# Performance work log

Measured on AMD Instinct MI355X. Metric: run time of the kernel, lower is better.

## Reference

```python
import jax, jax.numpy as jnp
import numpy as np

D_MODEL = 4096
D_HEAD = 128
N_ROPES = 4096
ROPE_COEF = 1.0


def _rope_buffers(n_ropes, d_head, rope_coef):
    # Faithful to torch _get_rotary_vectors (including the (i-1) exponent and
    # sin[:, 1::2] = cos(m) quirk).
    i = jnp.arange(d_head // 2, dtype=jnp.float32)
    theta = 10000.0 ** (-2.0 * (i - 1.0) / d_head)          # [d_head/2]
    m = jnp.arange(n_ropes, dtype=jnp.float32)[:, None] * theta * rope_coef  # [P, d/2]
    cosm, sinm = jnp.cos(m), jnp.sin(m)
    cos = jnp.repeat(cosm, 2, axis=-1)                       # even & odd = cos(m)
    sin = jnp.stack([-sinm, cosm], axis=-1).reshape(n_ropes, d_head)  # even=-sin, odd=cos
    return sin, cos


def setup_inputs() -> dict:
    key = jax.random.key(0)
    ks = jax.random.split(key, 7)
    x = jax.random.normal(ks[0], (4, 4096, D_MODEL), dtype=jnp.float32)
    w_q = jax.random.normal(ks[1], (D_HEAD, D_MODEL), dtype=jnp.float32) * 0.02
    w_k = jax.random.normal(ks[2], (D_HEAD, D_MODEL), dtype=jnp.float32) * 0.02
    w_v = jax.random.normal(ks[3], (D_HEAD, D_MODEL), dtype=jnp.float32) * 0.02
    b_q = jax.random.normal(ks[4], (D_HEAD,), dtype=jnp.float32) * 0.02
    b_k = jax.random.normal(ks[5], (D_HEAD,), dtype=jnp.float32) * 0.02
    b_v = jax.random.normal(ks[6], (D_HEAD,), dtype=jnp.float32) * 0.02
    sin, cos = _rope_buffers(N_ROPES, D_HEAD, ROPE_COEF)
    return {"x": x, "w_q": w_q, "b_q": b_q, "w_k": w_k, "b_k": b_k,
            "w_v": w_v, "b_v": b_v, "sin": sin, "cos": cos}


def reference(x, w_q, b_q, w_k, b_k, w_v, b_v, sin, cos):
    b, seq_len, d_model = x.shape
    q = jnp.einsum('bsd,hd->bsh', x, w_q) + b_q   # [B,S,d_head]
    k = jnp.einsum('bsd,hd->bsh', x, w_k) + b_k
    v = jnp.einsum('bsd,hd->bsh', x, w_v) + b_v
    c, s = cos[:seq_len], sin[:seq_len]
    # Torch in-place aliased swap puts the original ODD values into both
    # even and odd slots: [o0,o0,o1,o1,...].
    q_sw = jnp.repeat(q[..., 1::2], 2, axis=-1)
    k_sw = jnp.repeat(k[..., 1::2], 2, axis=-1)
    q_rot = q * c + q_sw * s
    k_rot = k * c + k_sw * s
    # causal scaled-dot-product attention (q/k/v are [B,S,d_head])
    scale = 1.0 / jnp.sqrt(jnp.float32(q.shape[-1]))
    scores = jnp.einsum('bqh,bkh->bqk', q_rot, k_rot) * scale
    causal = jnp.tril(jnp.ones((seq_len, seq_len), dtype=bool))
    scores = jnp.where(causal, scores, jnp.finfo(scores.dtype).min)
    attn = jax.nn.softmax(scores, axis=-1)
    return jnp.einsum('bqk,bkh->bqh', attn, v)
```

## Files before the change

kernel.cpp:

```cpp
#include <hip/hip_runtime.h>
#include <hip/hip_bf16.h>
#include <float.h>
#include <math.h>

typedef float f32x4 __attribute__((ext_vector_type(4)));
typedef short short8 __attribute__((ext_vector_type(8)));
typedef unsigned int uint32;

#define NB 4
#define SQ 4096
#define DM 4096
#define DH 128
#define LOG2E 1.44269504088896f
#define SCALE 0.0883883476483184f
#define SCL2 (SCALE * LOG2E)

__device__ __forceinline__ unsigned short f2bf(float f) {
  union { float f; unsigned u; } x; x.f = f;
  unsigned r = x.u + 0x7FFFu + ((x.u >> 16) & 1u);
  return (unsigned short)(r >> 16);
}

__device__ __forceinline__ uint2 cvt4(float4 f) {
  uint2 u;
  asm("v_cvt_pk_bf16_f32 %0, %1, %2" : "=v"(u.x) : "v"(f.x), "v"(f.y));
  asm("v_cvt_pk_bf16_f32 %0, %1, %2" : "=v"(u.y) : "v"(f.z), "v"(f.w));
  return u;
}

#define GLD16(g, l) __builtin_amdgcn_global_load_lds( \
    (const __attribute__((address_space(1))) void*)(g), \
    (__attribute__((address_space(3))) void*)(l), 16, 0, 0)

__global__ void cast_w_kernel(const float* __restrict__ wq, const float* __restrict__ wk,
                              const float* __restrict__ wv, const float* __restrict__ bq,
                              const float* __restrict__ bk, const float* __restrict__ bv,
                              unsigned short* __restrict__ wb, float* __restrict__ biasws) {
  int t = blockIdx.x * 256 + threadIdx.x;
  int base = t * 8;
  int n = base >> 12;
  int d = base & 4095;
  const float* src = (n < 128) ? (wq + (size_t)n * DM)
                   : (n < 256) ? (wk + (size_t)(n - 128) * DM)
                               : (wv + (size_t)(n - 256) * DM);
  float4 f0 = *(const float4*)(src + d);
  float4 f1 = *(const float4*)(src + d + 4);
  short8 v;
  v[0] = (short)f2bf(f0.x); v[1] = (short)f2bf(f0.y);
  v[2] = (short)f2bf(f0.z); v[3] = (short)f2bf(f0.w);
  v[4] = (short)f2bf(f1.x); v[5] = (short)f2bf(f1.y);
  v[6] = (short)f2bf(f1.z); v[7] = (short)f2bf(f1.w);
  *(short8*)(wb + base) = v;
  if (t < 384) biasws[t] = (t < 128) ? bq[t] : (t < 256) ? bk[t - 128] : bv[t - 256];
}

__global__ __launch_bounds__(256) void gemm_qkv_rope(
    const float* __restrict__ x, const unsigned short* __restrict__ wb,
    const float* __restrict__ biasws, const float* __restrict__ sing,
    const float* __restrict__ cosg, unsigned short* __restrict__ qb,
    unsigned short* __restrict__ kb, unsigned short* __restrict__ vt) {
  __shared__ __align__(16) short Alds[2 * 64 * 64];
  __shared__ __align__(16) short Blds[2 * 128 * 64];
  const int tid = threadIdx.x;
  const int l = tid & 63, w = tid >> 6;
  const int wm = w >> 1, wn = w & 1;
  const int l15 = l & 15, lg = l >> 4;
  const int bid = blockIdx.x;
  const int xcd = bid & 7, j = bid >> 3;
  const int mloc = j / 3, head = j - mloc * 3;
  const int m0 = (xcd * 32 + mloc) * 64;
  f32x4 acc[2][4] = {};
  const int ar0 = tid >> 4, ac4 = (tid & 15) * 4;
  const float* xsrc = x + (size_t)(m0 + ar0) * DM + ac4;
  const int achunk = (tid & 15) >> 1, ahalf = tid & 1;
  const int brow_ = tid >> 3, bchunk = tid & 7;
  const unsigned short* wbh = wb + (size_t)head * 128 * DM;
  float4 a00, a01, a02, a03, a10, a11, a12, a13;
  {
#pragma unroll
    for (int i = 0; i < 4; ++i) {
      float4 f = *(const float4*)(xsrc + (size_t)i * 16 * DM);
      int row = ar0 + i * 16;
      *(uint2*)&Alds[row * 64 + ((achunk ^ (row & 7)) * 8) + ahalf * 4] = cvt4(f);
    }
#pragma unroll
    for (int i = 0; i < 4; ++i) {
      int row = i * 32 + brow_;
      int slot = i * 256 + tid;
      GLD16(wbh + (size_t)row * DM + ((bchunk ^ (row & 7)) * 8), (char*)Blds + slot * 16);
    }
    a00 = *(const float4*)(xsrc + 64);
    a01 = *(const float4*)(xsrc + (size_t)16 * DM + 64);
    a02 = *(const float4*)(xsrc + (size_t)32 * DM + 64);
    a03 = *(const float4*)(xsrc + (size_t)48 * DM + 64);
  }
  auto giter = [&](int t, int CUR,
                   float4& n0, float4& n1, float4& n2, float4& n3,
                   float4& f0, float4& f1, float4& f2, float4& f3) {
    asm volatile("s_waitcnt vmcnt(4) lgkmcnt(0)" ::: "memory");
    __builtin_amdgcn_sched_barrier(0);
    __builtin_amdgcn_s_barrier();
    __builtin_amdgcn_sched_barrier(0);
    const int kB = (t + 1) * 64;
    char* bdst = (char*)Blds + (CUR ^ 1) * 16384;
#pragma unroll
    for (int i = 0; i < 4; ++i) {
      int row = i * 32 + brow_;
      int slot = i * 256 + tid;
      GLD16(wbh + (size_t)row * DM + kB + ((bchunk ^ (row & 7)) * 8), bdst + slot * 16);
    }
    __builtin_amdgcn_sched_barrier(0);
    const int kF = (t < 62) ? (t + 2) * 64 : 0;
    f0 = *(const float4*)(xsrc + kF);
    f1 = *(const float4*)(xsrc + (size_t)16 * DM + kF);
    f2 = *(const float4*)(xsrc + (size_t)32 * DM + kF);
    f3 = *(const float4*)(xsrc + (size_t)48 * DM + kF);
#pragma unroll
    for (int kc = 0; kc < 2; ++kc) {
      short8 af[2], bfr[4];
#pragma unroll
      for (int mi = 0; mi < 2; ++mi) {
        int r = wm * 32 + mi * 16 + l15;
        af[mi] = *(short8*)&Alds[CUR * 4096 + r * 64 + ((kc * 32 + lg * 8) ^ ((r & 7) << 3))];
      }
#pragma unroll
      for (int ni = 0; ni < 4; ++ni) {
        int r = wn * 64 + ni * 16 + l15;
        bfr[ni] = *(short8*)&Blds[CUR * 8192 + r * 64 + ((kc * 32 + lg * 8) ^ ((r & 7) << 3))];
      }
#pragma unroll
      for (int mi = 0; mi < 2; ++mi)
#pragma unroll
        for (int ni = 0; ni < 4; ++ni)
          acc[mi][ni] = __builtin_amdgcn_mfma_f32_16x16x32_bf16(af[mi], bfr[ni], acc[mi][ni], 0, 0, 0);
    }
    short* Adst = &Alds[(CUR ^ 1) * 4096];
    int r0 = ar0, r1 = ar0 + 16, r2 = ar0 + 32, r3 = ar0 + 48;
    *(uint2*)&Adst[r0 * 64 + ((achunk ^ (r0 & 7)) * 8) + ahalf * 4] = cvt4(n0);
    *(uint2*)&Adst[r1 * 64 + ((achunk ^ (r1 & 7)) * 8) + ahalf * 4] = cvt4(n1);
    *(uint2*)&Adst[r2 * 64 + ((achunk ^ (r2 & 7)) * 8) + ahalf * 4] = cvt4(n2);
    *(uint2*)&Adst[r3 * 64 + ((achunk ^ (r3 & 7)) * 8) + ahalf * 4] = cvt4(n3);
  };
#pragma unroll 1
  for (int t = 0; t < 62; t += 2) {
    giter(t, 0, a00, a01, a02, a03, a10, a11, a12, a13);
    giter(t + 1, 1, a10, a11, a12, a13, a00, a01, a02, a03);
  }
  giter(62, 0, a00, a01, a02, a03, a10, a11, a12, a13);
  {
    asm volatile("s_waitcnt vmcnt(0) lgkmcnt(0)" ::: "memory");
    __builtin_amdgcn_sched_barrier(0);
    __builtin_amdgcn_s_barrier();
    __builtin_amdgcn_sched_barrier(0);
#pragma unroll
    for (int kc = 0; kc < 2; ++kc) {
      short8 af[2], bfr[4];
#pragma unroll
      for (int mi = 0; mi < 2; ++mi) {
        int r = wm * 32 + mi * 16 + l15;
        af[mi] = *(short8*)&Alds[4096 + r * 64 + ((kc * 32 + lg * 8) ^ ((r & 7) << 3))];
      }
#pragma unroll
      for (int ni = 0; ni < 4; ++ni) {
        int r = wn * 64 + ni * 16 + l15;
        bfr[ni] = *(short8*)&Blds[8192 + r * 64 + ((kc * 32 + lg * 8) ^ ((r & 7) << 3))];
      }
#pragma unroll
      for (int mi = 0; mi < 2; ++mi)
#pragma unroll
        for (int ni = 0; ni < 4; ++ni)
          acc[mi][ni] = __builtin_amdgcn_mfma_f32_16x16x32_bf16(af[mi], bfr[ni], acc[mi][ni], 0, 0, 0);
    }
  }
  if (head == 2) {
    unsigned short* vtb = vt + (size_t)(m0 >> 12) * DH * SQ;
    const int srow = (m0 & (SQ - 1)) + wm * 32;
#pragma unroll
    for (int mi = 0; mi < 2; ++mi)
#pragma unroll
      for (int ni = 0; ni < 4; ++ni) {
        int h = wn * 64 + ni * 16 + l15;
        float bias = biasws[256 + h];
        f32x4 a = acc[mi][ni];
        float4 f;
        f.x = a[0] + bias; f.y = a[1] + bias; f.z = a[2] + bias; f.w = a[3] + bias;
        *(uint2*)&vtb[(size_t)h * SQ + srow + mi * 16 + lg * 4] = cvt4(f);
      }
  } else {
    unsigned short* dst = (head == 0) ? qb : kb;
#pragma unroll
    for (int mi = 0; mi < 2; ++mi)
#pragma unroll
      for (int ni = 0; ni < 4; ++ni) {
        int h = wn * 64 + ni * 16 + l15;
        float bias = biasws[head * 128 + h];
        f32x4 a = acc[mi][ni];
#pragma unroll
        for (int j2 = 0; j2 < 4; ++j2) {
          int row = m0 + wm * 32 + mi * 16 + lg * 4 + j2;
          float val = a[j2] + bias;
          int s = row & (SQ - 1);
          float cs = cosg[s * DH + h];
          float sn = sing[s * DH + h];
          float pr = __shfl_xor(val, 1, 64);
          float sw = (l & 1) ? val : pr;
          val = val * cs + sw * sn;
          dst[(size_t)row * DH + h] = f2bf(val);
        }
      }
  }
}

__global__ __launch_bounds__(256) void attn_kernel(
    const unsigned short* __restrict__ qb, const unsigned short* __restrict__ kb,
    const unsigned short* __restrict__ vt, float* __restrict__ out) {
  __shared__ __align__(16) short KV[4 * 8192];
  __shared__ __align__(16) short Plds4[4 * 1152];
  __shared__ __align__(16) float Mlds[64];
  __shared__ __align__(16) float Llds[64];
  __shared__ __align__(16) float Clds[64];
  const int tid = threadIdx.x;
  const int w = tid >> 6, l = tid & 63;
  const int qsub = w >> 1, ksp = w & 1;
  const int l15 = l & 15, lg = l >> 4;

  const int bi = blockIdx.x;
  const int slot = bi & 7, p5 = slot & 1, batch = slot >> 1;
  const int a = bi >> 3;
  const int t = (a & 1) ? (127 - p5 * 32 - (a >> 1)) : (p5 * 32 + (a >> 1));
  const int q0 = t * 32;
  const int qb0 = q0 + qsub * 16;
  const size_t bbase = (size_t)batch * SQ;
  const unsigned short* Kb = kb + bbase * DH;
  const unsigned short* Vtb = vt + (size_t)batch * DH * SQ;

  short* Kp = KV + ksp * 8192;
  short* Vp = KV + 16384 + ksp * 8192;
  short* Pw = Plds4 + w * 1152;

  const int ti = qsub * 64 + l;
  const int krow_ = ti >> 4, kc_ = ti & 15;
  const int vrow_ = ti >> 3, vc_ = ti & 7;

  short8 qf[4];
  {
    const unsigned short* qp = qb + (bbase + qb0 + l15) * DH + lg * 8;
#pragma unroll
    for (int kcd = 0; kcd < 4; ++kcd) qf[kcd] = *(const short8*)(qp + kcd * 32);
  }

  const int nsteps = (q0 + 32 + 63) >> 6;
  const int nsteps_w = (qb0 + 16 + 63) >> 6;
  const int max_nit = (nsteps + 1) >> 1;

  float m_r = -INFINITY, l_r = 0.f;
  f32x4 o[8] = {};

  for (int it = 0; it < max_nit; ++it) {
    const int st = it * 2 + ksp;
    const int kv0 = st * 64;
    if (st < nsteps) {
#pragma unroll
      for (int i = 0; i < 8; ++i) {
        int row = i * 8 + krow_;
        GLD16(Kb + (size_t)(kv0 + row) * DH + ((kc_ ^ (row & 15)) * 8),
              (char*)Kp + (i * 128 + ti) * 16);
      }
#pragma unroll
      for (int i = 0; i < 8; ++i) {
        int row = i * 16 + vrow_;
        GLD16(Vtb + (size_t)row * SQ + kv0 + ((vc_ ^ (row & 7)) * 8),
              (char*)Vp + (i * 128 + ti) * 16);
      }
    }
    asm volatile("s_waitcnt vmcnt(0)" ::: "memory");
    __builtin_amdgcn_s_barrier();

    if (st < nsteps_w) {
      f32x4 sf[4] = {};
      __builtin_amdgcn_s_setprio(1);
#pragma unroll
      for (int kcd = 0; kcd < 4; ++kcd)
#pragma unroll
        for (int ni = 0; ni < 4; ++ni) {
          int r = ni * 16 + l15;
          short8 kf = *(short8*)&Kp[r * 128 + (((kcd * 4 + lg) ^ (r & 15)) * 8)];
          sf[ni] = __builtin_amdgcn_mfma_f32_16x16x32_bf16(kf, qf[kcd], sf[ni], 0, 0, 0);
        }
      __builtin_amdgcn_s_setprio(0);

      float s[4][4];
      if (st == nsteps_w - 1) {
#pragma unroll
        for (int ni = 0; ni < 4; ++ni)
#pragma unroll
          for (int j = 0; j < 4; ++j) {
            float v = sf[ni][j] * SCL2;
            if (kv0 + ni * 16 + lg * 4 + j > qb0 + l15) v = -FLT_MAX;
            s[ni][j] = v;
          }
      } else {
#pragma unroll
        for (int ni = 0; ni < 4; ++ni)
#pragma unroll
          for (int j = 0; j < 4; ++j) s[ni][j] = sf[ni][j] * SCL2;
      }

      float tmx = s[0][0];
#pragma unroll
      for (int ni = 0; ni < 4; ++ni)
#pragma unroll
        for (int j = 0; j < 4; ++j) tmx = fmaxf(tmx, s[ni][j]);
      tmx = fmaxf(tmx, __shfl_xor(tmx, 16, 64));
      tmx = fmaxf(tmx, __shfl_xor(tmx, 32, 64));

      if (__any(tmx > m_r + 8.0f)) {
        float mnew = fmaxf(m_r, tmx);
        float corr = exp2f(m_r - mnew);
        if (l < 16) Clds[w * 16 + l] = corr;
        l_r *= corr; m_r = mnew;
        f32x4 c4 = *(f32x4*)&Clds[w * 16 + lg * 4];
#pragma unroll
        for (int nd = 0; nd < 8; ++nd)
#pragma unroll
          for (int j = 0; j < 4; ++j) o[nd][j] *= c4[j];
      }

      float rs = 0.f;
      float pp[4][4];
#pragma unroll
      for (int ni = 0; ni < 4; ++ni)
#pragma unroll
        for (int j = 0; j < 4; ++j) {
          pp[ni][j] = exp2f(s[ni][j] - m_r);
          rs += pp[ni][j];
        }
      rs += __shfl_xor(rs, 16, 64);
      rs += __shfl_xor(rs, 32, 64);
      l_r += rs;

#pragma unroll
      for (int ni = 0; ni < 4; ++ni) {
        uint32 lo, hi;
        asm volatile("v_cvt_pk_bf16_f32 %0, %1, %2" : "=v"(lo) : "v"(pp[ni][0]), "v"(pp[ni][1]));
        asm volatile("v_cvt_pk_bf16_f32 %0, %1, %2" : "=v"(hi) : "v"(pp[ni][2]), "v"(pp[ni][3]));
        uint2 u; u.x = lo; u.y = hi;
        *(uint2*)&Pw[l15 * 72 + ni * 16 + lg * 4] = u;
      }
      short8 pa0 = *(short8*)&Pw[l15 * 72 + lg * 8];
      short8 pa1 = *(short8*)&Pw[l15 * 72 + 32 + lg * 8];

      __builtin_amdgcn_s_setprio(1);
#pragma unroll
      for (int nd = 0; nd < 8; ++nd) {
        int r = nd * 16 + l15;
        short8 v0 = *(short8*)&Vp[r * 64 + ((lg ^ (r & 7)) * 8)];
        short8 v1 = *(short8*)&Vp[r * 64 + (((lg + 4) ^ (r & 7)) * 8)];
        o[nd] = __builtin_amdgcn_mfma_f32_16x16x32_bf16(pa0, v0, o[nd], 0, 0, 0);
        o[nd] = __builtin_amdgcn_mfma_f32_16x16x32_bf16(pa1, v1, o[nd], 0, 0, 0);
      }
      __builtin_amdgcn_s_setprio(0);
    }
    __builtin_amdgcn_s_barrier();
  }

  if (l < 16) { Mlds[w * 16 + l] = m_r; Llds[w * 16 + l] = l_r; }
  __syncthreads();
  float* Ob = (float*)KV;
#pragma unroll
  for (int nd = 0; nd < 8; ++nd)
#pragma unroll
    for (int j = 0; j < 4; ++j)
      Ob[w * 2112 + (lg * 4 + j) * 132 + nd * 16 + l15] = o[nd][j];
  __syncthreads();
  {
    const int w0 = qsub * 2, w1 = qsub * 2 + 1;
    float al0[4], al1[4], Lt[4];
#pragma unroll
    for (int j = 0; j < 4; ++j) {
      int q = lg * 4 + j;
      float ma = Mlds[w0 * 16 + q], mb = Mlds[w1 * 16 + q];
      float M = fmaxf(ma, mb);
      al0[j] = exp2f(ma - M); al1[j] = exp2f(mb - M);
      Lt[j] = al0[j] * Llds[w0 * 16 + q] + al1[j] * Llds[w1 * 16 + q];
    }
#pragma unroll
    for (int t2 = 0; t2 < 4; ++t2) {
      int nd = ksp * 4 + t2;
#pragma unroll
      for (int j = 0; j < 4; ++j) {
        int q = lg * 4 + j;
        float acc2 = al0[j] * Ob[w0 * 2112 + q * 132 + nd * 16 + l15]
                   + al1[j] * Ob[w1 * 2112 + q * 132 + nd * 16 + l15];
        out[(bbase + qb0 + q) * DH + nd * 16 + l15] = acc2 / Lt[j];
      }
    }
  }
}

extern "C" void kernel_launch(void* const* d_in, const int* in_sizes, int n_in,
                              void* d_out, int out_size, void* d_ws, size_t ws_size,
                              hipStream_t stream) {
  const float* x    = (const float*)d_in[0];
  const float* wq   = (const float*)d_in[1];
  const float* bq   = (const float*)d_in[2];
  const float* wk   = (const float*)d_in[3];
  const float* bk   = (const float*)d_in[4];
  const float* wv   = (const float*)d_in[5];
  const float* bv   = (const float*)d_in[6];
  const float* sing = (const float*)d_in[7];
  const float* cosg = (const float*)d_in[8];
  float* out = (float*)d_out;

  char* ws = (char*)d_ws;
  unsigned short* wb = (unsigned short*)ws;
  float* biasws = (float*)(ws + 3145728);
  unsigned short* qb = (unsigned short*)(ws + 3147264);
  unsigned short* kb = (unsigned short*)(ws + 3147264 + 4194304);
  unsigned short* vt = (unsigned short*)(ws + 3147264 + 2 * 4194304);

  cast_w_kernel<<<768, 256, 0, stream>>>(wq, wk, wv, bq, bk, bv, wb, biasws);
  gemm_qkv_rope<<<768, 256, 0, stream>>>(x, wb, biasws, sing, cosg, qb, kb, vt);
  attn_kernel<<<512, 256, 0, stream>>>(qb, kb, vt, out);
}
```

Before: 177.0 us.

## Rewrite QKV GEMM to load fragments directly from global into registers without LDS

The QKV projection GEMM drops its LDS double-buffered tiles. Each wave now loads its A (fp32 x) and B (bf16 weight) MFMA fragments straight from global memory into a three-deep register ring, converting A to bf16 in registers. The grid becomes 1536 blocks of 128 threads, each covering 128 rows by 32 output columns, with no block barriers. This is meant to remove LDS traffic and synchronisation, but it raises register pressure and global/L2 traffic because tiles are no longer shared across waves.

```diff
diff --git a/kernel.cpp b/kernel.cpp
--- a/kernel.cpp
+++ b/kernel.cpp
@@ -26,6 +26,17 @@
   asm("v_cvt_pk_bf16_f32 %0, %1, %2" : "=v"(u.x) : "v"(f.x), "v"(f.y));
   asm("v_cvt_pk_bf16_f32 %0, %1, %2" : "=v"(u.y) : "v"(f.z), "v"(f.w));
   return u;
+}
+
+__device__ __forceinline__ short8 pack8(f32x4 u, f32x4 v) {
+  uint32 r0, r1, r2, r3;
+  asm("v_cvt_pk_bf16_f32 %0, %1, %2" : "=v"(r0) : "v"(u[0]), "v"(u[1]));
+  asm("v_cvt_pk_bf16_f32 %0, %1, %2" : "=v"(r1) : "v"(u[2]), "v"(u[3]));
+  asm("v_cvt_pk_bf16_f32 %0, %1, %2" : "=v"(r2) : "v"(v[0]), "v"(v[1]));
+  asm("v_cvt_pk_bf16_f32 %0, %1, %2" : "=v"(r3) : "v"(v[2]), "v"(v[3]));
+  union { uint32 w[4]; short8 s; } z;
+  z.w[0] = r0; z.w[1] = r1; z.w[2] = r2; z.w[3] = r3;
+  return z.s;
 }
 
 #define GLD16(g, l) __builtin_amdgcn_global_load_lds( \
@@ -54,132 +65,83 @@
   if (t < 384) biasws[t] = (t < 128) ? bq[t] : (t < 256) ? bk[t - 128] : bv[t - 256];
 }
 
-__global__ __launch_bounds__(256) void gemm_qkv_rope(
+struct ABuf { f32x4 r[8]; };
+struct BBuf { short8 b[2]; };
+
+__global__ __launch_bounds__(128, 2) void gemm_qkv_rope(
     const float* __restrict__ x, const unsigned short* __restrict__ wb,
     const float* __restrict__ biasws, const float* __restrict__ sing,
     const float* __restrict__ cosg, unsigned short* __restrict__ qb,
     unsigned short* __restrict__ kb, unsigned short* __restrict__ vt) {
-  __shared__ __align__(16) short Alds[2 * 64 * 64];
-  __shared__ __align__(16) short Blds[2 * 128 * 64];
   const int tid = threadIdx.x;
   const int l = tid & 63, w = tid >> 6;
-  const int wm = w >> 1, wn = w & 1;
   const int l15 = l & 15, lg = l >> 4;
+
   const int bid = blockIdx.x;
-  const int xcd = bid & 7, j = bid >> 3;
-  const int mloc = j / 3, head = j - mloc * 3;
-  const int m0 = (xcd * 32 + mloc) * 64;
-  f32x4 acc[2][4] = {};
-  const int ar0 = tid >> 4, ac4 = (tid & 15) * 4;
-  const float* xsrc = x + (size_t)(m0 + ar0) * DM + ac4;
-  const int achunk = (tid & 15) >> 1, ahalf = tid & 1;
-  const int brow_ = tid >> 3, bchunk = tid & 7;
-  const unsigned short* wbh = wb + (size_t)head * 128 * DM;
-  float4 a00, a01, a02, a03, a10, a11, a12, a13;
-  {
-#pragma unroll
-    for (int i = 0; i < 4; ++i) {
-      float4 f = *(const float4*)(xsrc + (size_t)i * 16 * DM);
-      int row = ar0 + i * 16;
-      *(uint2*)&Alds[row * 64 + ((achunk ^ (row & 7)) * 8) + ahalf * 4] = cvt4(f);
-    }
-#pragma unroll
-    for (int i = 0; i < 4; ++i) {
-      int row = i * 32 + brow_;
-      int slot = i * 256 + tid;
-      GLD16(wbh + (size_t)row * DM + ((bchunk ^ (row & 7)) * 8), (char*)Blds + slot * 16);
-    }
-    a00 = *(const float4*)(xsrc + 64);
-    a01 = *(const float4*)(xsrc + (size_t)16 * DM + 64);
-    a02 = *(const float4*)(xsrc + (size_t)32 * DM + 64);
-    a03 = *(const float4*)(xsrc + (size_t)48 * DM + 64);
-  }
-  auto giter = [&](int t, int CUR,
-                   float4& n0, float4& n1, float4& n2, float4& n3,
-                   float4& f0, float4& f1, float4& f2, float4& f3) {
-    asm volatile("s_waitcnt vmcnt(4) lgkmcnt(0)" ::: "memory");
-    __builtin_amdgcn_sched_barrier(0);
-    __builtin_amdgcn_s_barrier();
-    __builtin_amdgcn_sched_barrier(0);
-    const int kB = (t + 1) * 64;
-    char* bdst = (char*)Blds + (CUR ^ 1) * 16384;
-#pragma unroll
-    for (int i = 0; i < 4; ++i) {
-      int row = i * 32 + brow_;
-      int slot = i * 256 + tid;
-      GLD16(wbh + (size_t)row * DM + kB + ((bchunk ^ (row & 7)) * 8), bdst + slot * 16);
-    }
-    __builtin_amdgcn_sched_barrier(0);
-    const int kF = (t < 62) ? (t + 2) * 64 : 0;
-    f0 = *(const float4*)(xsrc + kF);
-    f1 = *(const float4*)(xsrc + (size_t)16 * DM + kF);
-    f2 = *(const float4*)(xsrc + (size_t)32 * DM + kF);
-    f3 = *(const float4*)(xsrc + (size_t)48 * DM + kF);
-#pragma unroll
-    for (int kc = 0; kc < 2; ++kc) {
-      short8 af[2], bfr[4];
-#pragma unroll
-      for (int mi = 0; mi < 2; ++mi) {
-        int r = wm * 32 + mi * 16 + l15;
-        af[mi] = *(short8*)&Alds[CUR * 4096 + r * 64 + ((kc * 32 + lg * 8) ^ ((r & 7) << 3))];
-      }
-#pragma unroll
-      for (int ni = 0; ni < 4; ++ni) {
-        int r = wn * 64 + ni * 16 + l15;
-        bfr[ni] = *(short8*)&Blds[CUR * 8192 + r * 64 + ((kc * 32 + lg * 8) ^ ((r & 7) << 3))];
-      }
-#pragma unroll
-      for (int mi = 0; mi < 2; ++mi)
-#pragma unroll
-        for (int ni = 0; ni < 4; ++ni)
-          acc[mi][ni] = __builtin_amdgcn_mfma_f32_16x16x32_bf16(af[mi], bfr[ni], acc[mi][ni], 0, 0, 0);
-    }
-    short* Adst = &Alds[(CUR ^ 1) * 4096];
-    int r0 = ar0, r1 = ar0 + 16, r2 = ar0 + 32, r3 = ar0 + 48;
-    *(uint2*)&Adst[r0 * 64 + ((achunk ^ (r0 & 7)) * 8) + ahalf * 4] = cvt4(n0);
-    *(uint2*)&Adst[r1 * 64 + ((achunk ^ (r1 & 7)) * 8) + ahalf * 4] = cvt4(n1);
-    *(uint2*)&Adst[r2 * 64 + ((achunk ^ (r2 & 7)) * 8) + ahalf * 4] = cvt4(n2);
-    *(uint2*)&Adst[r3 * 64 + ((achunk ^ (r3 & 7)) * 8) + ahalf * 4] = cvt4(n3);
+  const int xcd = bid & 7, q = bid >> 3;
+  const int mloc = q / 12, nsl = q - mloc * 12;
+  const int m0 = (xcd * 16 + mloc) * 128 + w * 64;
+  const int n0 = nsl * 32;
+  const int head = nsl >> 2;
+
+  const float* xsrc = x + (size_t)(m0 + l15) * DM + lg * 8;
+  const unsigned short* bsrc = wb + (size_t)(n0 + l15) * DM + lg * 8;
+
+  f32x4 acc[4][2] = {};
+  ABuf A0, A1, A2;
+  BBuf B0, B1, B2;
+
+  auto ldA = [&](ABuf& A, int k) {
+#pragma unroll
+    for (int mi = 0; mi < 4; ++mi) {
+      A.r[2 * mi]     = *(const f32x4*)(xsrc + (size_t)mi * 16 * DM + k);
+      A.r[2 * mi + 1] = *(const f32x4*)(xsrc + (size_t)mi * 16 * DM + k + 4);
+    }
   };
+  auto ldB = [&](BBuf& B, int k) {
+    B.b[0] = *(const short8*)(bsrc + k);
+    B.b[1] = *(const short8*)(bsrc + (size_t)16 * DM + k);
+  };
+
+  ldA(A0, 0);  ldB(B0, 0);
+  ldA(A1, 32); ldB(B1, 32);
+  ldA(A2, 64); ldB(B2, 64);
+
+  auto body = [&](ABuf& A, BBuf& B, int t, bool re) {
+    short8 af[4];
+#pragma unroll
+    for (int mi = 0; mi < 4; ++mi) af[mi] = pack8(A.r[2 * mi], A.r[2 * mi + 1]);
+    short8 b0 = B.b[0], b1 = B.b[1];
+    if (re) {
+      const int kn = ((t + 3) & 127) * 32;
+      ldA(A, kn);
+      ldB(B, kn);
+    }
+#pragma unroll
+    for (int mi = 0; mi < 4; ++mi) {
+      acc[mi][0] = __builtin_amdgcn_mfma_f32_16x16x32_bf16(af[mi], b0, acc[mi][0], 0, 0, 0);
+      acc[mi][1] = __builtin_amdgcn_mfma_f32_16x16x32_bf16(af[mi], b1, acc[mi][1], 0, 0, 0);
+    }
+  };
+
 #pragma unroll 1
-  for (int t = 0; t < 62; t += 2) {
-    giter(t, 0, a00, a01, a02, a03, a10, a11, a12, a13);
-    giter(t + 1, 1, a10, a11, a12, a13, a00, a01, a02, a03);
-  }
-  giter(62, 0, a00, a01, a02, a03, a10, a11, a12, a13);
-  {
-    asm volatile("s_waitcnt vmcnt(0) lgkmcnt(0)" ::: "memory");
-    __builtin_amdgcn_sched_barrier(0);
-    __builtin_amdgcn_s_barrier();
-    __builtin_amdgcn_sched_barrier(0);
-#pragma unroll
-    for (int kc = 0; kc < 2; ++kc) {
-      short8 af[2], bfr[4];
-#pragma unroll
-      for (int mi = 0; mi < 2; ++mi) {
-        int r = wm * 32 + mi * 16 + l15;
-        af[mi] = *(short8*)&Alds[4096 + r * 64 + ((kc * 32 + lg * 8) ^ ((r & 7) << 3))];
-      }
-#pragma unroll
-      for (int ni = 0; ni < 4; ++ni) {
-        int r = wn * 64 + ni * 16 + l15;
-        bfr[ni] = *(short8*)&Blds[8192 + r * 64 + ((kc * 32 + lg * 8) ^ ((r & 7) << 3))];
-      }
-#pragma unroll
-      for (int mi = 0; mi < 2; ++mi)
-#pragma unroll
-        for (int ni = 0; ni < 4; ++ni)
-          acc[mi][ni] = __builtin_amdgcn_mfma_f32_16x16x32_bf16(af[mi], bfr[ni], acc[mi][ni], 0, 0, 0);
-    }
-  }
+  for (int tt = 0; tt < 42; ++tt) {
+    const int t = tt * 3;
+    body(A0, B0, t, true);
+    body(A1, B1, t + 1, true);
+    body(A2, B2, t + 2, true);
+  }
+  body(A0, B0, 126, false);
+  body(A1, B1, 127, false);
+
   if (head == 2) {
     unsigned short* vtb = vt + (size_t)(m0 >> 12) * DH * SQ;
-    const int srow = (m0 & (SQ - 1)) + wm * 32;
-#pragma unroll
-    for (int mi = 0; mi < 2; ++mi)
-#pragma unroll
-      for (int ni = 0; ni < 4; ++ni) {
-        int h = wn * 64 + ni * 16 + l15;
+    const int srow = m0 & (SQ - 1);
+#pragma unroll
+    for (int mi = 0; mi < 4; ++mi)
+#pragma unroll
+      for (int ni = 0; ni < 2; ++ni) {
+        int h = (n0 & 127) + ni * 16 + l15;
         float bias = biasws[256 + h];
         f32x4 a = acc[mi][ni];
         float4 f;
@@ -189,15 +151,15 @@
   } else {
     unsigned short* dst = (head == 0) ? qb : kb;
 #pragma unroll
-    for (int mi = 0; mi < 2; ++mi)
-#pragma unroll
-      for (int ni = 0; ni < 4; ++ni) {
-        int h = wn * 64 + ni * 16 + l15;
+    for (int mi = 0; mi < 4; ++mi)
+#pragma unroll
+      for (int ni = 0; ni < 2; ++ni) {
+        int h = (n0 & 127) + ni * 16 + l15;
         float bias = biasws[head * 128 + h];
         f32x4 a = acc[mi][ni];
 #pragma unroll
         for (int j2 = 0; j2 < 4; ++j2) {
-          int row = m0 + wm * 32 + mi * 16 + lg * 4 + j2;
+          int row = m0 + mi * 16 + lg * 4 + j2;
           float val = a[j2] + bias;
           int s = row & (SQ - 1);
           float cs = cosg[s * DH + h];
@@ -378,21 +340,21 @@
     float al0[4], al1[4], Lt[4];
 #pragma unroll
     for (int j = 0; j < 4; ++j) {
-      int q = lg * 4 + j;
-      float ma = Mlds[w0 * 16 + q], mb = Mlds[w1 * 16 + q];
+      int q2 = lg * 4 + j;
+      float ma = Mlds[w0 * 16 + q2], mb = Mlds[w1 * 16 + q2];
       float M = fmaxf(ma, mb);
       al0[j] = exp2f(ma - M); al1[j] = exp2f(mb - M);
-      Lt[j] = al0[j] * Llds[w0 * 16 + q] + al1[j] * Llds[w1 * 16 + q];
+      Lt[j] = al0[j] * Llds[w0 * 16 + q2] + al1[j] * Llds[w1 * 16 + q2];
     }
 #pragma unroll
     for (int t2 = 0; t2 < 4; ++t2) {
       int nd = ksp * 4 + t2;
 #pragma unroll
       for (int j = 0; j < 4; ++j) {
-        int q = lg * 4 + j;
-        float acc2 = al0[j] * Ob[w0 * 2112 + q * 132 + nd * 16 + l15]
-                   + al1[j] * Ob[w1 * 2112 + q * 132 + nd * 16 + l15];
-        out[(bbase + qb0 + q) * DH + nd * 16 + l15] = acc2 / Lt[j];
+        int q2 = lg * 4 + j;
+        float acc2 = al0[j] * Ob[w0 * 2112 + q2 * 132 + nd * 16 + l15]
+                   + al1[j] * Ob[w1 * 2112 + q2 * 132 + nd * 16 + l15];
+        out[(bbase + qb0 + q2) * DH + nd * 16 + l15] = acc2 / Lt[j];
       }
     }
   }
@@ -420,6 +382,6 @@
   unsigned short* vt = (unsigned short*)(ws + 3147264 + 2 * 4194304);
 
   cast_w_kernel<<<768, 256, 0, stream>>>(wq, wk, wv, bq, bk, bv, wb, biasws);
-  gemm_qkv_rope<<<768, 256, 0, stream>>>(x, wb, biasws, sing, cosg, qb, kb, vt);
+  gemm_qkv_rope<<<1536, 128, 0, stream>>>(x, wb, biasws, sing, cosg, qb, kb, vt);
   attn_kernel<<<512, 256, 0, stream>>>(qb, kb, vt, out);
 }
```

Result: slower. 513.9 us (+190.4%).
